# Performance work log

Hardware: AMD Instinct MI355X
Metric: run time of the kernel (lower is better)

## Reference

```python
import jax, jax.numpy as jnp
import numpy as np

MODEL_DIM = 1024
NUM_HEADS = 16
HEAD_DIM = MODEL_DIM // NUM_HEADS
ROPE_BASE = 10000.0


def apply_rope_full(x):
    # RoPE applied over the FULL model_dim (before head split), interleaved pairs.
    B, S, D = x.shape
    half = D // 2
    inv_freq = 1.0 / (ROPE_BASE ** (jnp.arange(half, dtype=x.dtype) / half))  # [half]
    ang = jnp.arange(S, dtype=x.dtype)[:, None] * inv_freq[None, :]           # [S, half]
    cos, sin = jnp.cos(ang), jnp.sin(ang)
    x1 = x[..., 0::2]  # [B,S,half]
    x2 = x[..., 1::2]
    r1 = x1 * cos - x2 * sin
    r2 = x1 * sin + x2 * cos
    # re-interleave
    return jnp.stack([r1, r2], axis=-1).reshape(B, S, D)


def setup_inputs() -> dict:
    key = jax.random.key(0)
    ks = jax.random.split(key, 9)
    B, S, D = 4, 2048, MODEL_DIM
    sc = 1.0 / np.sqrt(D)
    inp = {
        "X": jax.random.normal(ks[0], (B, S, D), dtype=jnp.float32),
        "Wq": jax.random.normal(ks[1], (D, D), dtype=jnp.float32) * sc,
        "bq": jnp.zeros((D,), dtype=jnp.float32),
        "Wk": jax.random.normal(ks[2], (D, D), dtype=jnp.float32) * sc,
        "bk": jnp.zeros((D,), dtype=jnp.float32),
        "Wv": jax.random.normal(ks[3], (D, D), dtype=jnp.float32) * sc,
        "bv": jnp.zeros((D,), dtype=jnp.float32),
        "Wo": jax.random.normal(ks[4], (D, D), dtype=jnp.float32) * sc,
        "bo": jnp.zeros((D,), dtype=jnp.float32),
    }
    return inp


def reference(X, Wq, bq, Wk, bk, Wv, bv, Wo, bo):
    B, S, D = X.shape
    H, hd = NUM_HEADS, HEAD_DIM
    q = apply_rope_full(X @ Wq + bq)  # [B,S,D], RoPE on full dim as in source
    k = apply_rope_full(X @ Wk + bk)
    v = X @ Wv + bv
    # split heads (contiguous slices d1:d2 == reshape to [B,S,H,hd])
    qh = q.reshape(B, S, H, hd)
    kh = k.reshape(B, S, H, hd)
    vh = v.reshape(B, S, H, hd)
    scale = 1.0 / jnp.sqrt(jnp.asarray(hd, dtype=X.dtype))
    scores = jnp.einsum("bqhd,bkhd->bhqk", qh, kh) * scale  # [B,H,S,S]
    causal = jnp.tril(jnp.ones((S, S), dtype=bool))
    scores = jnp.where(causal[None, None], scores, -jnp.inf)
    weights = jax.nn.softmax(scores, axis=-1)
    attn = jnp.einsum("bhqk,bkhd->bqhd", weights, vh).reshape(B, S, D)
    return attn @ Wo + bo
```

## Files before the change

### kernel.cpp

```cpp
#include <hip/hip_runtime.h>

typedef unsigned short u16;
typedef unsigned int   u32;
typedef __attribute__((ext_vector_type(4))) float f32x4;
typedef __attribute__((ext_vector_type(8))) short short8;

#define MODEL_DIM 1024
#define SEQ 2048
#define BATCH 4
#define NHEAD 16
#define HDIM 64
#define MTOT (BATCH*SEQ)
#define ELEMS ((size_t)MTOT*MODEL_DIM)

__device__ __forceinline__ u16 f2bf(float f) {
    u32 u = __float_as_uint(f);
    u = (u + 0x7fffu + ((u >> 16) & 1u)) >> 16;
    return (u16)u;
}
__device__ __forceinline__ u32 pack2(float a, float b) {
    return (u32)f2bf(a) | ((u32)f2bf(b) << 16);
}
__device__ __forceinline__ float bflo(u32 u) { return __uint_as_float(u << 16); }
__device__ __forceinline__ float bfhi(u32 u) { return __uint_as_float(u & 0xffff0000u); }
__device__ __forceinline__ u32 cvtpk(float lo, float hi) {
    u32 r;
    asm("v_cvt_pk_bf16_f32 %0, %1, %2" : "=v"(r) : "v"(lo), "v"(hi));
    return r;
}

#define GLOAD16(g, l) __builtin_amdgcn_global_load_lds(                        \
        (const __attribute__((address_space(1))) unsigned int*)(g),            \
        (__attribute__((address_space(3))) unsigned int*)(l), 16, 0, 0)

__global__ void cast_x_k(const float* __restrict__ X, u16* __restrict__ Xb) {
    size_t i = ((size_t)blockIdx.x * 256 + threadIdx.x) * 4;
    float4 v = *(const float4*)(X + i);
    uint2 o; o.x = pack2(v.x, v.y); o.y = pack2(v.z, v.w);
    *(uint2*)(Xb + i) = o;
}

__global__ void transw_k(const float* __restrict__ Wq, const float* __restrict__ Wk,
                         const float* __restrict__ Wv, const float* __restrict__ Wo,
                         u16* __restrict__ Wt) {
    __shared__ float tile[32][33];
    int z = blockIdx.z;
    const float* W = (z == 0) ? Wq : (z == 1) ? Wk : (z == 2) ? Wv : Wo;
    int k0 = blockIdx.y * 32, n0 = blockIdx.x * 32;
    int x = threadIdx.x, y = threadIdx.y;
    for (int i = 0; i < 4; ++i)
        tile[y + i * 8][x] = W[(size_t)(k0 + y + i * 8) * MODEL_DIM + n0 + x];
    __syncthreads();
    u16* out = Wt + ((size_t)z << 20);
    for (int i = 0; i < 4; ++i)
        out[(size_t)(n0 + y + i * 8) * MODEL_DIM + k0 + x] = f2bf(tile[x][y + i * 8]);
}

template<int MODE>
__global__ __launch_bounds__(256) void gemm128_k(
        const u16* __restrict__ A, const u16* __restrict__ Wt,
        u16* __restrict__ Qb, u16* __restrict__ Kb, u16* __restrict__ Vb,
        float* __restrict__ outO,
        const float* __restrict__ bq, const float* __restrict__ bk,
        const float* __restrict__ bv, const float* __restrict__ bo) {
    __shared__ __align__(16) u16 As[128 * 32];
    __shared__ __align__(16) u16 Bs[128 * 32];
    const int tid  = threadIdx.x;
    const int wave = tid >> 6, lane = tid & 63;
    const int l15  = lane & 15, quad = lane >> 4;
    const int wm = (wave & 1) * 64, wn = (wave >> 1) * 64;
    const int m0 = blockIdx.x * 128;
    const int n0 = blockIdx.y * 128;

    const u16* bbase;
    if (MODE == 0) {
        int region = n0 >> 10;
        bbase = Wt + ((size_t)region << 20) + (size_t)(n0 & 1023) * MODEL_DIM;
    } else {
        bbase = Wt + ((size_t)3 << 20) + (size_t)n0 * MODEL_DIM;
    }
    const u16* abase = A + (size_t)m0 * MODEL_DIM;

    f32x4 acc[4][4] = {};
    const int r0 = tid >> 2, kc0 = (tid & 3) * 8;
    const u16* ga = abase + (size_t)r0 * MODEL_DIM + kc0;
    const u16* gb = bbase + (size_t)r0 * MODEL_DIM + kc0;
    u16* la0 = &As[tid * 8];
    u16* la1 = &As[2048 + tid * 8];
    u16* lb0 = &Bs[tid * 8];
    u16* lb1 = &Bs[2048 + tid * 8];

    for (int k0 = 0; k0 < MODEL_DIM; k0 += 32) {
        GLOAD16(ga + k0, la0);
        GLOAD16(ga + (size_t)64 * MODEL_DIM + k0, la1);
        GLOAD16(gb + k0, lb0);
        GLOAD16(gb + (size_t)64 * MODEL_DIM + k0, lb1);
        __syncthreads();
        short8 af[4], bf[4];
        for (int i = 0; i < 4; ++i)
            af[i] = *(const short8*)(&As[(wm + i * 16 + l15) * 32 + quad * 8]);
        for (int i = 0; i < 4; ++i)
            bf[i] = *(const short8*)(&Bs[(wn + i * 16 + l15) * 32 + quad * 8]);
        for (int mi = 0; mi < 4; ++mi)
            for (int ni = 0; ni < 4; ++ni)
                acc[mi][ni] = __builtin_amdgcn_mfma_f32_16x16x32_bf16(
                                  af[mi], bf[ni], acc[mi][ni], 0, 0, 0);
        __syncthreads();
    }

    if (MODE == 0) {
        const int region = n0 >> 10;
        const float* bias = (region == 0) ? bq : (region == 1) ? bk : bv;
        u16* dst = (region == 0) ? Qb : (region == 1) ? Kb : Vb;
        if (region < 2) {
            const float qsc = (region == 0) ? 0.125f : 1.0f;
            const float cfr = -0.017989922f;
            float invf[4];
            for (int ni = 0; ni < 4; ++ni) {
                int c = (n0 + wn + ni * 16 + l15) & 1023;
                invf[ni] = __expf((float)(c >> 1) * cfr);
            }
            const float sgn = (l15 & 1) ? 1.0f : -1.0f;
            for (int mi = 0; mi < 4; ++mi)
                for (int r = 0; r < 4; ++r) {
                    size_t rowg = (size_t)(m0 + wm + mi * 16 + quad * 4 + r);
                    float fs = (float)(int)(rowg & 2047);
                    for (int ni = 0; ni < 4; ++ni) {
                        int c = (n0 + wn + ni * 16 + l15) & 1023;
                        float v = acc[mi][ni][r] + bias[c];
                        float mate = __shfl_xor(v, 1, 64);
                        float sn, cs;
                        __sincosf(fs * invf[ni], &sn, &cs);
                        float o = (v * cs + sgn * mate * sn) * qsc;
                        dst[rowg * MODEL_DIM + c] = f2bf(o);
                    }
                }
        } else {
            for (int mi = 0; mi < 4; ++mi)
                for (int r = 0; r < 4; ++r) {
                    size_t rowg = (size_t)(m0 + wm + mi * 16 + quad * 4 + r);
                    for (int ni = 0; ni < 4; ++ni) {
                        int col = (n0 + wn + ni * 16 + l15) & 1023;
                        dst[rowg * MODEL_DIM + col] = f2bf(acc[mi][ni][r] + bias[col]);
                    }
                }
        }
    } else {
        for (int mi = 0; mi < 4; ++mi)
            for (int r = 0; r < 4; ++r) {
                size_t rowg = (size_t)(m0 + wm + mi * 16 + quad * 4 + r);
                for (int ni = 0; ni < 4; ++ni) {
                    int colg = n0 + wn + ni * 16 + l15;
                    outO[rowg * MODEL_DIM + colg] = acc[mi][ni][r] + bo[colg];
                }
            }
    }
}

__global__ __launch_bounds__(256) void vt_k(const u32* __restrict__ Vb32,
                                            u32* __restrict__ VT32) {
    __shared__ u32 tile[64 * 33];
    int bh = blockIdx.y, b = bh >> 4, h = bh & 15;
    int s0 = blockIdx.x * 64;
    int t = threadIdx.x;
    for (int it = 0; it < 8; ++it) {
        int idx = it * 256 + t;
        int s = idx >> 5, dc = idx & 31;
        tile[s * 33 + dc] = Vb32[(size_t)(b * SEQ + s0 + s) * (MODEL_DIM / 2)
                                 + h * (HDIM / 2) + dc];
    }
    __syncthreads();
    for (int it = 0; it < 8; ++it) {
        int idx = it * 256 + t;
        int d = idx >> 5, sc = idx & 31;
        u32 w0 = tile[(2 * sc) * 33 + (d >> 1)];
        u32 w1 = tile[(2 * sc + 1) * 33 + (d >> 1)];
        u32 val = (d & 1) ? ((w0 >> 16) | (w1 & 0xffff0000u))
                          : ((w0 & 0xffffu) | (w1 << 16));
        VT32[(size_t)(bh * HDIM + d) * (SEQ / 2) + (s0 >> 1) + sc] = val;
    }
}

__global__ __launch_bounds__(256, 2) void attn_k(const u16* __restrict__ Qb,
                                                 const u16* __restrict__ Kb,
                                                 const u32* __restrict__ VT32,
                                                 u16* __restrict__ Ob) {
    __shared__ __align__(16) u16 Ks[2][64 * 64];
    __shared__ __align__(16) u16 Vs[2][64 * 64];
    __shared__ __align__(16) u16 Pl[4 * 32 * 72];
    const int tid  = threadIdx.x;
    const int wave = tid >> 6, lane = tid & 63;
    const int l15  = lane & 15, quad = lane >> 4;
    const int j = blockIdx.x;
    const int h = blockIdx.y, b = blockIdx.z;
    u16* pw = &Pl[wave * 32 * 72];

    const int key0 = tid >> 3;
    const int c8   = (tid & 7) * 8;
    const int c4   = (tid & 7) * 4;
    const int lko  = key0 * 64 + (((tid & 7) ^ (key0 & 7)) * 8);
    const u16* kgp = Kb + (size_t)(b * SEQ) * MODEL_DIM + h * HDIM;
    const u32* vgp = VT32 + (size_t)((b * NHEAD + h) * HDIM) * (SEQ / 2);

    int bufc = 0;
    for (int pp = 0; pp < 2; ++pp) {
        const int qt = pp ? j : 15 - j;
        const int q0 = qt * 128;
        const int qbase = q0 + wave * 32;

        short8 qfr[2][2];
        for (int qf = 0; qf < 2; ++qf)
            for (int ks = 0; ks < 2; ++ks)
                qfr[qf][ks] = *(const short8*)(Qb
                    + (size_t)(b * SEQ + qbase + qf * 16 + l15) * MODEL_DIM
                    + h * HDIM + ks * 32 + quad * 8);

        float m_i[2] = {-1e30f, -1e30f}, l_i[2] = {0.f, 0.f};
        f32x4 o_acc[4][2] = {};

        const int nkt = (q0 + 128) >> 6;
        uint4 kr0 = *(const uint4*)(kgp + (size_t)key0 * MODEL_DIM + c8);
        uint4 kr1 = *(const uint4*)(kgp + (size_t)(key0 + 32) * MODEL_DIM + c8);
        uint4 vr0 = *(const uint4*)(vgp + (size_t)key0 * (SEQ / 2) + c4);
        uint4 vr1 = *(const uint4*)(vgp + (size_t)(key0 + 32) * (SEQ / 2) + c4);

        for (int kt = 0; kt < nkt; ++kt) {
            const int k0 = kt * 64;
            u16* ksb = Ks[bufc];
            u16* vsb = Vs[bufc];
            *(uint4*)(&ksb[lko])        = kr0;
            *(uint4*)(&ksb[lko + 2048]) = kr1;
            *(uint4*)(&vsb[lko])        = vr0;
            *(uint4*)(&vsb[lko + 2048]) = vr1;
            __syncthreads();

            if (kt + 1 < nkt) {
                const int kn = k0 + 64;
                kr0 = *(const uint4*)(kgp + (size_t)(kn + key0) * MODEL_DIM + c8);
                kr1 = *(const uint4*)(kgp + (size_t)(kn + key0 + 32) * MODEL_DIM + c8);
                vr0 = *(const uint4*)(vgp + (size_t)key0 * (SEQ / 2) + (kn >> 1) + c4);
                vr1 = *(const uint4*)(vgp + (size_t)(key0 + 32) * (SEQ / 2)
                                      + (kn >> 1) + c4);
            }

            if (k0 <= qbase + 31) {
                f32x4 s[4][2] = {};
                for (int ks = 0; ks < 2; ++ks) {
                    short8 kfr[4];
                    for (int kf = 0; kf < 4; ++kf)
                        kfr[kf] = *(const short8*)(&ksb[(kf * 16 + l15) * 64
                                      + (((ks * 4 + quad) ^ (l15 & 7)) * 8)]);
                    for (int kf = 0; kf < 4; ++kf)
                        for (int qf = 0; qf < 2; ++qf)
                            s[kf][qf] = __builtin_amdgcn_mfma_f32_16x16x32_bf16(
                                            kfr[kf], qfr[qf][ks], s[kf][qf], 0, 0, 0);
                }
                for (int qf = 0; qf < 2; ++qf) {
                    int qg = qbase + qf * 16 + l15;
                    if (k0 + 63 > qbase + qf * 16) {
                        for (int kf = 0; kf < 4; ++kf)
                            for (int r = 0; r < 4; ++r)
                                if (k0 + kf * 16 + quad * 4 + r > qg)
                                    s[kf][qf][r] = -1e30f;
                    }
                    float rmax = s[0][qf][0];
                    for (int kf = 0; kf < 4; ++kf)
                        for (int r = 0; r < 4; ++r) rmax = fmaxf(rmax, s[kf][qf][r]);
                    rmax = fmaxf(rmax, __shfl_xor(rmax, 16, 64));
                    rmax = fmaxf(rmax, __shfl_xor(rmax, 32, 64));
                    if (!__all(rmax <= m_i[qf] + 8.0f)) {
                        float mn = fmaxf(m_i[qf], rmax);
                        float alpha = __expf(m_i[qf] - mn);
                        m_i[qf] = mn;
                        l_i[qf] *= alpha;
                        for (int dt = 0; dt < 4; ++dt)
                            for (int r = 0; r < 4; ++r) o_acc[dt][qf][r] *= alpha;
                    }
                    float mref = m_i[qf];
                    float psum = 0.f;
                    for (int kf = 0; kf < 4; ++kf)
                        for (int r = 0; r < 4; ++r) {
                            float p = __expf(s[kf][qf][r] - mref);
                            s[kf][qf][r] = p;
                            psum += p;
                        }
                    psum += __shfl_xor(psum, 16, 64);
                    psum += __shfl_xor(psum, 32, 64);
                    l_i[qf] += psum;
                    for (int kf = 0; kf < 4; ++kf) {
                        uint2 w;
                        w.x = cvtpk(s[kf][qf][0], s[kf][qf][1]);
                        w.y = cvtpk(s[kf][qf][2], s[kf][qf][3]);
                        *(uint2*)(&pw[(qf * 16 + l15) * 72 + kf * 16 + quad * 4]) = w;
                    }
                }
                for (int ks = 0; ks < 2; ++ks) {
                    short8 pfr[2], vfr[4];
                    for (int qf = 0; qf < 2; ++qf)
                        pfr[qf] = *(const short8*)(&pw[(qf * 16 + l15) * 72
                                                       + ks * 32 + quad * 8]);
                    for (int dt = 0; dt < 4; ++dt)
                        vfr[dt] = *(const short8*)(&vsb[(dt * 16 + l15) * 64
                                      + (((ks * 4 + quad) ^ (l15 & 7)) * 8)]);
                    for (int dt = 0; dt < 4; ++dt)
                        for (int qf = 0; qf < 2; ++qf)
                            o_acc[dt][qf] = __builtin_amdgcn_mfma_f32_16x16x32_bf16(
                                                vfr[dt], pfr[qf], o_acc[dt][qf], 0, 0, 0);
                }
            }
            bufc ^= 1;
        }

        for (int qf = 0; qf < 2; ++qf) {
            float rl = 1.f / l_i[qf];
            int q = qbase + qf * 16 + l15;
            for (int dt = 0; dt < 4; ++dt) {
                uint2 w;
                w.x = cvtpk(o_acc[dt][qf][0] * rl, o_acc[dt][qf][1] * rl);
                w.y = cvtpk(o_acc[dt][qf][2] * rl, o_acc[dt][qf][3] * rl);
                *(uint2*)(&Ob[(size_t)(b * SEQ + q) * MODEL_DIM
                              + h * HDIM + dt * 16 + quad * 4]) = w;
            }
        }
    }
}

extern "C" void kernel_launch(void* const* d_in, const int* in_sizes, int n_in,
                              void* d_out, int out_size, void* d_ws, size_t ws_size,
                              hipStream_t stream) {
    const float* X  = (const float*)d_in[0];
    const float* Wq = (const float*)d_in[1];
    const float* bq = (const float*)d_in[2];
    const float* Wk = (const float*)d_in[3];
    const float* bk = (const float*)d_in[4];
    const float* Wv = (const float*)d_in[5];
    const float* bv = (const float*)d_in[6];
    const float* Wo = (const float*)d_in[7];
    const float* bo = (const float*)d_in[8];
    float* out = (float*)d_out;

    char* ws = (char*)d_ws;
    u16* Xb   = (u16*)ws;
    u16* Ob   = (u16*)ws;
    u16* Wt   = (u16*)(ws + 16777216);
    u16* Qb   = (u16*)(ws + 25165824);
    u16* Kb   = (u16*)(ws + 41943040);
    u16* Vb   = (u16*)(ws + 58720256);
    u32* VT32 = (u32*)(ws + 75497472);

    cast_x_k<<<dim3(ELEMS / 1024), dim3(256), 0, stream>>>(X, Xb);
    transw_k<<<dim3(32, 32, 4), dim3(32, 8), 0, stream>>>(Wq, Wk, Wv, Wo, Wt);
    gemm128_k<0><<<dim3(64, 24), dim3(256), 0, stream>>>(Xb, Wt, Qb, Kb, Vb, nullptr,
                                                         bq, bk, bv, nullptr);
    vt_k<<<dim3(32, 64), dim3(256), 0, stream>>>((const u32*)Vb, VT32);
    attn_k<<<dim3(8, 16, 4), dim3(256), 0, stream>>>(Qb, Kb, VT32, Ob);
    gemm128_k<1><<<dim3(64, 8), dim3(256), 0, stream>>>(Ob, Wt, nullptr, nullptr,
                                                        nullptr, out,
                                                        nullptr, nullptr, nullptr, bo);
}
```

Measured before the change: 279.3 us.

## Fuse prep kernels, write V transposed from GEMM epilogue, use exp2 softmax

```diff
diff --git a/kernel.cpp b/kernel.cpp
--- a/kernel.cpp
+++ b/kernel.cpp
@@ -21,33 +21,43 @@
 __device__ __forceinline__ u32 pack2(float a, float b) {
     return (u32)f2bf(a) | ((u32)f2bf(b) << 16);
 }
-__device__ __forceinline__ float bflo(u32 u) { return __uint_as_float(u << 16); }
-__device__ __forceinline__ float bfhi(u32 u) { return __uint_as_float(u & 0xffff0000u); }
 __device__ __forceinline__ u32 cvtpk(float lo, float hi) {
     u32 r;
     asm("v_cvt_pk_bf16_f32 %0, %1, %2" : "=v"(r) : "v"(lo), "v"(hi));
     return r;
 }
+__device__ __forceinline__ float exp2a(float x) {
+    float r;
+    asm("v_exp_f32 %0, %1" : "=v"(r) : "v"(x));
+    return r;
+}
 
 #define GLOAD16(g, l) __builtin_amdgcn_global_load_lds(                        \
         (const __attribute__((address_space(1))) unsigned int*)(g),            \
         (__attribute__((address_space(3))) unsigned int*)(l), 16, 0, 0)
 
-__global__ void cast_x_k(const float* __restrict__ X, u16* __restrict__ Xb) {
-    size_t i = ((size_t)blockIdx.x * 256 + threadIdx.x) * 4;
-    float4 v = *(const float4*)(X + i);
-    uint2 o; o.x = pack2(v.x, v.y); o.y = pack2(v.z, v.w);
-    *(uint2*)(Xb + i) = o;
-}
-
-__global__ void transw_k(const float* __restrict__ Wq, const float* __restrict__ Wk,
-                         const float* __restrict__ Wv, const float* __restrict__ Wo,
-                         u16* __restrict__ Wt) {
+__global__ __launch_bounds__(256) void prep_k(const float* __restrict__ X,
+                                              u16* __restrict__ Xb,
+                                              const float* __restrict__ Wq,
+                                              const float* __restrict__ Wk,
+                                              const float* __restrict__ Wv,
+                                              const float* __restrict__ Wo,
+                                              u16* __restrict__ Wt) {
+    const int bid = blockIdx.x, t = threadIdx.x;
+    if (bid < 8192) {
+        size_t i = ((size_t)bid * 256 + t) * 4;
+        float4 v = *(const float4*)(X + i);
+        uint2 o; o.x = pack2(v.x, v.y); o.y = pack2(v.z, v.w);
+        *(uint2*)(Xb + i) = o;
+        return;
+    }
     __shared__ float tile[32][33];
-    int z = blockIdx.z;
+    const int bid2 = bid - 8192;
+    const int z = bid2 >> 10, rem = bid2 & 1023;
+    const int by = rem >> 5, bx = rem & 31;
     const float* W = (z == 0) ? Wq : (z == 1) ? Wk : (z == 2) ? Wv : Wo;
-    int k0 = blockIdx.y * 32, n0 = blockIdx.x * 32;
-    int x = threadIdx.x, y = threadIdx.y;
+    const int k0 = by * 32, n0 = bx * 32;
+    const int x = t & 31, y = t >> 5;
     for (int i = 0; i < 4; ++i)
         tile[y + i * 8][x] = W[(size_t)(k0 + y + i * 8) * MODEL_DIM + n0 + x];
     __syncthreads();
@@ -59,12 +69,13 @@
 template<int MODE>
 __global__ __launch_bounds__(256) void gemm128_k(
         const u16* __restrict__ A, const u16* __restrict__ Wt,
-        u16* __restrict__ Qb, u16* __restrict__ Kb, u16* __restrict__ Vb,
+        u16* __restrict__ Qb, u16* __restrict__ Kb, u32* __restrict__ VT,
         float* __restrict__ outO,
         const float* __restrict__ bq, const float* __restrict__ bk,
         const float* __restrict__ bv, const float* __restrict__ bo) {
-    __shared__ __align__(16) u16 As[128 * 32];
-    __shared__ __align__(16) u16 Bs[128 * 32];
+    __shared__ __align__(16) u16 smem[(MODE == 0) ? 128 * 130 : 128 * 64];
+    u16* As = smem;
+    u16* Bs = smem + 4096;
     const int tid  = threadIdx.x;
     const int wave = tid >> 6, lane = tid & 63;
     const int l15  = lane & 15, quad = lane >> 4;
@@ -110,10 +121,10 @@
 
     if (MODE == 0) {
         const int region = n0 >> 10;
-        const float* bias = (region == 0) ? bq : (region == 1) ? bk : bv;
-        u16* dst = (region == 0) ? Qb : (region == 1) ? Kb : Vb;
         if (region < 2) {
-            const float qsc = (region == 0) ? 0.125f : 1.0f;
+            const float* bias = (region == 0) ? bq : bk;
+            u16* dst = (region == 0) ? Qb : Kb;
+            const float qsc = (region == 0) ? 0.125f * 1.44269504f : 1.0f;
             const float cfr = -0.017989922f;
             float invf[4];
             for (int ni = 0; ni < 4; ++ni) {
@@ -136,14 +147,27 @@
                     }
                 }
         } else {
+            u16* Ts = smem;
             for (int mi = 0; mi < 4; ++mi)
                 for (int r = 0; r < 4; ++r) {
-                    size_t rowg = (size_t)(m0 + wm + mi * 16 + quad * 4 + r);
+                    int rl = wm + mi * 16 + quad * 4 + r;
                     for (int ni = 0; ni < 4; ++ni) {
-                        int col = (n0 + wn + ni * 16 + l15) & 1023;
-                        dst[rowg * MODEL_DIM + col] = f2bf(acc[mi][ni][r] + bias[col]);
-                    }
-                }
+                        int cl = wn + ni * 16 + l15;
+                        Ts[cl * 130 + rl] = f2bf(acc[mi][ni][r]
+                                                 + bv[(n0 & 1023) + cl]);
+                    }
+                }
+            __syncthreads();
+            const int b_ = m0 >> 11;
+            const int srow0 = (m0 & 2047) >> 1;
+            const int h0 = (n0 & 1023) >> 6;
+            u32* vtb = VT + (size_t)((b_ * NHEAD + h0) * HDIM) * (SEQ / 2);
+            for (int it = 0; it < 32; ++it) {
+                int idx = it * 256 + tid;
+                int dl = idx >> 6, sc = idx & 63;
+                u32 val = *(const u32*)&Ts[dl * 130 + 2 * sc];
+                vtb[(size_t)dl * (SEQ / 2) + srow0 + sc] = val;
+            }
         }
     } else {
         for (int mi = 0; mi < 4; ++mi)
@@ -154,30 +178,6 @@
                     outO[rowg * MODEL_DIM + colg] = acc[mi][ni][r] + bo[colg];
                 }
             }
-    }
-}
-
-__global__ __launch_bounds__(256) void vt_k(const u32* __restrict__ Vb32,
-                                            u32* __restrict__ VT32) {
-    __shared__ u32 tile[64 * 33];
-    int bh = blockIdx.y, b = bh >> 4, h = bh & 15;
-    int s0 = blockIdx.x * 64;
-    int t = threadIdx.x;
-    for (int it = 0; it < 8; ++it) {
-        int idx = it * 256 + t;
-        int s = idx >> 5, dc = idx & 31;
-        tile[s * 33 + dc] = Vb32[(size_t)(b * SEQ + s0 + s) * (MODEL_DIM / 2)
-                                 + h * (HDIM / 2) + dc];
-    }
-    __syncthreads();
-    for (int it = 0; it < 8; ++it) {
-        int idx = it * 256 + t;
-        int d = idx >> 5, sc = idx & 31;
-        u32 w0 = tile[(2 * sc) * 33 + (d >> 1)];
-        u32 w1 = tile[(2 * sc + 1) * 33 + (d >> 1)];
-        u32 val = (d & 1) ? ((w0 >> 16) | (w1 & 0xffff0000u))
-                          : ((w0 & 0xffffu) | (w1 << 16));
-        VT32[(size_t)(bh * HDIM + d) * (SEQ / 2) + (s0 >> 1) + sc] = val;
     }
 }
 
@@ -263,14 +263,20 @@
                                 if (k0 + kf * 16 + quad * 4 + r > qg)
                                     s[kf][qf][r] = -1e30f;
                     }
-                    float rmax = s[0][qf][0];
-                    for (int kf = 0; kf < 4; ++kf)
-                        for (int r = 0; r < 4; ++r) rmax = fmaxf(rmax, s[kf][qf][r]);
+                    float t0 = fmaxf(fmaxf(s[0][qf][0], s[0][qf][1]),
+                                     fmaxf(s[0][qf][2], s[0][qf][3]));
+                    float t1 = fmaxf(fmaxf(s[1][qf][0], s[1][qf][1]),
+                                     fmaxf(s[1][qf][2], s[1][qf][3]));
+                    float t2 = fmaxf(fmaxf(s[2][qf][0], s[2][qf][1]),
+                                     fmaxf(s[2][qf][2], s[2][qf][3]));
+                    float t3 = fmaxf(fmaxf(s[3][qf][0], s[3][qf][1]),
+                                     fmaxf(s[3][qf][2], s[3][qf][3]));
+                    float rmax = fmaxf(fmaxf(t0, t1), fmaxf(t2, t3));
                     rmax = fmaxf(rmax, __shfl_xor(rmax, 16, 64));
                     rmax = fmaxf(rmax, __shfl_xor(rmax, 32, 64));
                     if (!__all(rmax <= m_i[qf] + 8.0f)) {
                         float mn = fmaxf(m_i[qf], rmax);
-                        float alpha = __expf(m_i[qf] - mn);
+                        float alpha = exp2a(m_i[qf] - mn);
                         m_i[qf] = mn;
                         l_i[qf] *= alpha;
                         for (int dt = 0; dt < 4; ++dt)
@@ -280,7 +286,7 @@
                     float psum = 0.f;
                     for (int kf = 0; kf < 4; ++kf)
                         for (int r = 0; r < 4; ++r) {
-                            float p = __expf(s[kf][qf][r] - mref);
+                            float p = exp2a(s[kf][qf][r] - mref);
                             s[kf][qf][r] = p;
                             psum += p;
                         }
@@ -345,14 +351,11 @@
     u16* Wt   = (u16*)(ws + 16777216);
     u16* Qb   = (u16*)(ws + 25165824);
     u16* Kb   = (u16*)(ws + 41943040);
-    u16* Vb   = (u16*)(ws + 58720256);
     u32* VT32 = (u32*)(ws + 75497472);
 
-    cast_x_k<<<dim3(ELEMS / 1024), dim3(256), 0, stream>>>(X, Xb);
-    transw_k<<<dim3(32, 32, 4), dim3(32, 8), 0, stream>>>(Wq, Wk, Wv, Wo, Wt);
-    gemm128_k<0><<<dim3(64, 24), dim3(256), 0, stream>>>(Xb, Wt, Qb, Kb, Vb, nullptr,
-                                                         bq, bk, bv, nullptr);
-    vt_k<<<dim3(32, 64), dim3(256), 0, stream>>>((const u32*)Vb, VT32);
+    prep_k<<<dim3(12288), dim3(256), 0, stream>>>(X, Xb, Wq, Wk, Wv, Wo, Wt);
+    gemm128_k<0><<<dim3(64, 24), dim3(256), 0, stream>>>(Xb, Wt, Qb, Kb, VT32,
+                                                         nullptr, bq, bk, bv, nullptr);
     attn_k<<<dim3(8, 16, 4), dim3(256), 0, stream>>>(Qb, Kb, VT32, Ob);
     gemm128_k<1><<<dim3(64, 8), dim3(256), 0, stream>>>(Ob, Wt, nullptr, nullptr,
                                                         nullptr, out,
```

Result: faster. 271.6 us (-2.8%).
